# Kernel optimization log

Hardware: AMD Instinct MI355X
Metric: run time of the kernel (lower is better)

## Reference

```python
import jax, jax.numpy as jnp
import numpy as np

N_NODES = 100000
N_EDGES = 1600000
HID = 128
MAX_Z = 1000
N_GRAPHS = 1000
N_LAYERS = 3


def setup_inputs() -> dict:
    key = jax.random.key(0)
    ks = jax.random.split(key, 10)
    z = jax.random.randint(ks[0], (N_NODES,), 0, MAX_Z)
    edge_index = jax.random.randint(ks[1], (2, N_EDGES), 0, N_NODES)
    batch = jnp.sort(jax.random.randint(ks[2], (N_NODES,), 0, N_GRAPHS))
    s = 1.0 / np.sqrt(HID)
    z_emb = jax.random.normal(ks[3], (MAX_Z, HID), jnp.float32)
    Wl = jax.random.normal(ks[4], (N_LAYERS, HID, HID), jnp.float32) * s
    bl = jnp.zeros((N_LAYERS, HID), jnp.float32)
    Wr = jax.random.normal(ks[5], (N_LAYERS, HID, HID), jnp.float32) * s
    lin1_w = jax.random.normal(ks[6], (HID, HID), jnp.float32) * s
    lin1_b = jnp.zeros((HID,), jnp.float32)
    lin2_w = jax.random.normal(ks[7], (1, HID), jnp.float32) * s
    lin2_b = jnp.zeros((1,), jnp.float32)
    return dict(z=z, edge_index=edge_index, batch=batch, num_graphs=N_GRAPHS,
                z_emb=z_emb, Wl=Wl, bl=bl, Wr=Wr,
                lin1_w=lin1_w, lin1_b=lin1_b, lin2_w=lin2_w, lin2_b=lin2_b)


def _sage_conv(x, src, dst, deg_inv, Wl_i, bl_i, Wr_i):
    # PyG SAGEConv (default): out = lin_l(mean_{j in N(i)} x_j) + lin_r(x_i)
    agg = jax.ops.segment_sum(x[src], dst, num_segments=x.shape[0]) * deg_inv[:, None]
    return agg @ Wl_i.T + bl_i + x @ Wr_i.T


def reference(z, edge_index, batch, num_graphs, z_emb, Wl, bl, Wr, lin1_w, lin1_b, lin2_w, lin2_b):
    x = z_emb[z]  # z.ndim == 1 -> z_emb.ndim == 2, no sum branch
    src, dst = edge_index[0], edge_index[1]
    n = x.shape[0]
    deg = jax.ops.segment_sum(jnp.ones((src.shape[0],), x.dtype), dst, num_segments=n)
    deg_inv = 1.0 / jnp.maximum(deg, 1.0)  # mean aggregation; empty neighborhoods -> 0
    for i in range(Wl.shape[0] - 1):
        x = jax.nn.relu(_sage_conv(x, src, dst, deg_inv, Wl[i], bl[i], Wr[i]))
        # dropout is identity in eval mode
    x = _sage_conv(x, src, dst, deg_inv, Wl[-1], bl[-1], Wr[-1])
    # batch is sorted; first occurrence of each graph id == searchsorted
    center = jnp.searchsorted(batch, jnp.arange(num_graphs))
    h = x[center] * x[center + 1]
    h = jax.nn.relu(h @ lin1_w.T + lin1_b)
    return h @ lin2_w.T + lin2_b  # [num_graphs, 1]
```

## Files before the change

### kernel.cpp

```cpp
#include <hip/hip_runtime.h>
#include <hip/hip_bf16.h>
#include <cstdint>

#define HID 128
#define GM 128
#define SCAN_CHUNK 2048
#define NBIN 512
#define CHUNK 2048
#define MAXHI 1024

typedef __attribute__((ext_vector_type(8))) short bf16x8;
typedef __attribute__((ext_vector_type(4))) float f32x4;

__device__ __forceinline__ unsigned short f2bf(float f) {
    union { __hip_bfloat16 h; unsigned short u; } c;
    c.h = __float2bfloat16(f);
    return c.u;
}
__device__ __forceinline__ float bf2f(unsigned short u) {
    union { unsigned int i; float f; } c;
    c.i = ((unsigned int)u) << 16;
    return c.f;
}
__device__ __forceinline__ unsigned int pack2(unsigned short a, unsigned short b) {
    return (unsigned int)a | ((unsigned int)b << 16);
}
__device__ __forceinline__ bf16x8 ld_frag(const unsigned int* p) {
    union { uint4 u; bf16x8 f; } c;
    c.u = *(const uint4*)p;
    return c.f;
}

__device__ __forceinline__ int block_scan_excl(int v, int t, int* wtot, int* tot) {
    int lane = t & 63, wv = t >> 6;
    int incl = v;
#pragma unroll
    for (int off = 1; off < 64; off <<= 1) {
        int u = __shfl_up(incl, off);
        if (lane >= off) incl += u;
    }
    if (lane == 63) wtot[wv] = incl;
    __syncthreads();
    int woff = 0;
    for (int w = 0; w < wv; ++w) woff += wtot[w];
    if (tot) *tot = wtot[0] + wtot[1] + wtot[2] + wtot[3];
    __syncthreads();
    return woff + incl - v;
}

__global__ __launch_bounds__(256) void k_hist(const int* __restrict__ dst,
                                              int* __restrict__ hist, int n_edges) {
    __shared__ int h[NBIN];
    int t = threadIdx.x;
    h[t] = 0; h[t + 256] = 0;
    __syncthreads();
    int base = blockIdx.x * CHUNK;
#pragma unroll
    for (int j = 0; j < CHUNK / 256; ++j) {
        int e = base + j * 256 + t;
        if (e < n_edges) atomicAdd(&h[dst[e] & (NBIN - 1)], 1);
    }
    __syncthreads();
    hist[(size_t)blockIdx.x * NBIN + t] = h[t];
    hist[(size_t)blockIdx.x * NBIN + t + 256] = h[t + 256];
}

__global__ __launch_bounds__(256) void k_colscan(int* __restrict__ hist,
                                                 int* __restrict__ bintotal, int B) {
    __shared__ int wtot[4];
    int k = blockIdx.x, t = threadIdx.x;
    int run = 0;
    for (int base = 0; base < B; base += 256) {
        int b = base + t;
        int v = (b < B) ? hist[(size_t)b * NBIN + k] : 0;
        int tot;
        int excl = block_scan_excl(v, t, wtot, &tot);
        if (b < B) hist[(size_t)b * NBIN + k] = run + excl;
        run += tot;
    }
    if (t == 0) bintotal[k] = run;
}

__global__ __launch_bounds__(256) void k_binbase(const int* __restrict__ bintotal,
                                                 int* __restrict__ binbase) {
    __shared__ int wtot[4];
    int t = threadIdx.x;
    int a0 = bintotal[2 * t], a1 = bintotal[2 * t + 1];
    int excl = block_scan_excl(a0 + a1, t, wtot, nullptr);
    binbase[2 * t] = excl;
    binbase[2 * t + 1] = excl + a0;
    if (t == 255) binbase[NBIN] = excl + a0 + a1;
}

__global__ __launch_bounds__(256) void k_route(const int* __restrict__ src,
                                               const int* __restrict__ dst,
                                               const int* __restrict__ histex,
                                               const int* __restrict__ binbase,
                                               int2* __restrict__ ebuf, int n_edges) {
    __shared__ int h2[NBIN];
    __shared__ int basel[NBIN];
    int t = threadIdx.x;
    h2[t] = 0; h2[t + 256] = 0;
    basel[t]       = binbase[t]       + histex[(size_t)blockIdx.x * NBIN + t];
    basel[t + 256] = binbase[t + 256] + histex[(size_t)blockIdx.x * NBIN + t + 256];
    __syncthreads();
    int base = blockIdx.x * CHUNK;
#pragma unroll
    for (int j = 0; j < CHUNK / 256; ++j) {
        int e = base + j * 256 + t;
        if (e < n_edges) {
            int d = dst[e], s = src[e];
            int bin = d & (NBIN - 1);
            int r = atomicAdd(&h2[bin], 1);
            ebuf[basel[bin] + r] = make_int2(s, d);
        }
    }
}

__global__ __launch_bounds__(256) void k_group(const int2* __restrict__ ebuf,
                                               const int* __restrict__ binbase,
                                               const int* __restrict__ z,
                                               int2* __restrict__ csr2,
                                               int* __restrict__ start, int* __restrict__ deg,
                                               int n_nodes) {
    __shared__ int hh[MAXHI];
    __shared__ int cur[MAXHI];
    __shared__ int wtot[4];
    int k = blockIdx.x, t = threadIdx.x;
    int rs = binbase[k], re = binbase[k + 1];
#pragma unroll
    for (int j = 0; j < MAXHI / 256; ++j) hh[t + j * 256] = 0;
    __syncthreads();
    for (int i = rs + t; i < re; i += 256)
        atomicAdd(&hh[ebuf[i].y >> 9], 1);
    __syncthreads();
    int idx = t * 4;
    int a0 = hh[idx], a1 = hh[idx + 1], a2 = hh[idx + 2], a3 = hh[idx + 3];
    int excl = block_scan_excl(a0 + a1 + a2 + a3, t, wtot, nullptr);
    int e0 = excl, e1 = e0 + a0, e2 = e1 + a1, e3 = e2 + a2;
    cur[idx] = e0; cur[idx + 1] = e1; cur[idx + 2] = e2; cur[idx + 3] = e3;
    int ee[4] = {e0, e1, e2, e3};
    int aa[4] = {a0, a1, a2, a3};
#pragma unroll
    for (int j = 0; j < 4; ++j) {
        int node = ((idx + j) << 9) | k;
        if (node < n_nodes) {
            start[node] = rs + ee[j];
            deg[node] = aa[j];
        }
    }
    __syncthreads();
    for (int i = rs + t; i < re; i += 256) {
        int2 sd = ebuf[i];
        int r = atomicAdd(&cur[sd.y >> 9], 1);
        csr2[rs + r] = make_int2(sd.x, z[sd.x]);
    }
}

__global__ void k_scan1(const int* __restrict__ v_in, int* __restrict__ partials, int n) {
    __shared__ int sm[256];
    int t = threadIdx.x;
    int base = blockIdx.x * SCAN_CHUNK + t * 8;
    int s = 0;
#pragma unroll
    for (int j = 0; j < 8; ++j) { int i = base + j; if (i < n) s += v_in[i]; }
    sm[t] = s;
    __syncthreads();
    for (int off = 128; off > 0; off >>= 1) {
        if (t < off) sm[t] += sm[t + off];
        __syncthreads();
    }
    if (t == 0) partials[blockIdx.x] = sm[0];
}

__global__ void k_scan2(int* partials, int nchunks, int* total) {
    int lane = threadIdx.x;
    int v = (lane < nchunks) ? partials[lane] : 0;
#pragma unroll
    for (int off = 1; off < 64; off <<= 1) {
        int u = __shfl_up(v, off);
        if (lane >= off) v += u;
    }
    if (total && lane == nchunks - 1) *total = v;
    int ex = __shfl_up(v, 1);
    if (lane == 0) ex = 0;
    if (lane < nchunks) partials[lane] = ex;
}

__global__ void k_compact(const int* __restrict__ flag, const int* __restrict__ partials,
                          int* __restrict__ remap, int* __restrict__ nodes2, int n) {
    __shared__ int wtot[4];
    int t = threadIdx.x;
    int lane = t & 63, wv = t >> 6;
    int base = blockIdx.x * SCAN_CHUNK + t * 8;
    int v[8];
    int ts = 0;
#pragma unroll
    for (int j = 0; j < 8; ++j) { int i = base + j; v[j] = (i < n) ? flag[i] : 0; ts += v[j]; }
    int incl = ts;
#pragma unroll
    for (int off = 1; off < 64; off <<= 1) {
        int u = __shfl_up(incl, off);
        if (lane >= off) incl += u;
    }
    if (lane == 63) wtot[wv] = incl;
    __syncthreads();
    int woff = 0;
    for (int w = 0; w < wv; ++w) woff += wtot[w];
    int run = partials[blockIdx.x] + woff + (incl - ts);
#pragma unroll
    for (int j = 0; j < 8; ++j) {
        int i = base + j;
        if (i < n) {
            remap[i] = run;
            if (v[j]) nodes2[run] = i;
        }
        run += v[j];
    }
}

__global__ void k_zlr(const float* __restrict__ z_emb, const float* __restrict__ Wl,
                      const float* __restrict__ Wr, const float* __restrict__ bl,
                      float* __restrict__ zl, float* __restrict__ zr, int max_z) {
    __shared__ float row[HID];
    int r = blockIdx.x;
    if (r >= max_z) return;
    int t = threadIdx.x;
    if (t < HID) row[t] = z_emb[(size_t)r * HID + t];
    __syncthreads();
    int d = t & 127;
    const float* w = (t < 128 ? Wl : Wr) + (size_t)d * HID;
    float acc = 0.f;
#pragma unroll
    for (int k4 = 0; k4 < HID / 4; ++k4) {
        float4 wv = *(const float4*)(w + k4 * 4);
        float4 hv = *(const float4*)&row[k4 * 4];
        acc += wv.x * hv.x + wv.y * hv.y + wv.z * hv.z + wv.w * hv.w;
    }
    if (t < 128) zl[(size_t)r * HID + d] = acc;
    else         zr[(size_t)r * HID + d] = acc + bl[d];
}

__global__ void k_flag(const int* __restrict__ sel, const int* __restrict__ start,
                       const int* __restrict__ deg,
                       const int2* __restrict__ csr2, int* __restrict__ flag, int n_sel) {
    int r = (blockIdx.x * blockDim.x + threadIdx.x) >> 6;
    int lane = threadIdx.x & 63;
    if (r >= n_sel) return;
    int node = sel[r];
    if (lane == 0) flag[node] = 1;
    int s = start[node], e = s + deg[node];
    for (int i = s + lane; i < e; i += 64) flag[csr2[i].x] = 1;
}

__global__ void k_selremap(const int* __restrict__ sel, const int* __restrict__ remap,
                           int* __restrict__ selr, int n_sel) {
    int i = blockIdx.x * blockDim.x + threadIdx.x;
    if (i < n_sel) selr[i] = remap[sel[i]];
}

template<int MODE>
__global__ __launch_bounds__(256) void k_agg(const float* __restrict__ xv_,
                      float* __restrict__ aggout,
                      const int* __restrict__ start, const int* __restrict__ deg,
                      const int2* __restrict__ csr2,
                      const int* __restrict__ idxmap, const int* __restrict__ remap,
                      const int* __restrict__ z, const float* __restrict__ zr,
                      int n_host, const int* __restrict__ n_dev) {
    int nw_total = gridDim.x * 4;
    int w0 = blockIdx.x * 4 + (threadIdx.x >> 6);
    int lane = threadIdx.x & 63;
    int n = n_dev ? *n_dev : n_host;
    int half = lane >> 5;
    int col = lane & 31;
    const float4* xv = (const float4*)xv_;
    for (int r = w0; r < n; r += nw_total) {
        int node = (MODE == 1) ? r : idxmap[r];
        int s = start[node];
        int dg = deg[node];
        int e = s + dg;
        float4 a0 = {0.f,0.f,0.f,0.f}, a1 = {0.f,0.f,0.f,0.f};
        float4 a2 = {0.f,0.f,0.f,0.f}, a3 = {0.f,0.f,0.f,0.f};
        int i = s + half;
        for (; i + 6 < e; i += 8) {
            int2 c0 = csr2[i];
            int2 c1 = csr2[i + 2];
            int2 c2 = csr2[i + 4];
            int2 c3 = csr2[i + 6];
            int s0 = (MODE == 1) ? c0.y : c0.x;
            int s1 = (MODE == 1) ? c1.y : c1.x;
            int s2 = (MODE == 1) ? c2.y : c2.x;
            int s3 = (MODE == 1) ? c3.y : c3.x;
            if (MODE == 3) { s0 = remap[s0]; s1 = remap[s1]; s2 = remap[s2]; s3 = remap[s3]; }
            float4 v0 = xv[(size_t)s0 * 32 + col];
            float4 v1 = xv[(size_t)s1 * 32 + col];
            float4 v2 = xv[(size_t)s2 * 32 + col];
            float4 v3 = xv[(size_t)s3 * 32 + col];
            a0.x += v0.x; a0.y += v0.y; a0.z += v0.z; a0.w += v0.w;
            a1.x += v1.x; a1.y += v1.y; a1.z += v1.z; a1.w += v1.w;
            a2.x += v2.x; a2.y += v2.y; a2.z += v2.z; a2.w += v2.w;
            a3.x += v3.x; a3.y += v3.y; a3.z += v3.z; a3.w += v3.w;
        }
        for (; i < e; i += 2) {
            int2 c0 = csr2[i];
            int s0 = (MODE == 1) ? c0.y : c0.x;
            if (MODE == 3) s0 = remap[s0];
            float4 v0 = xv[(size_t)s0 * 32 + col];
            a0.x += v0.x; a0.y += v0.y; a0.z += v0.z; a0.w += v0.w;
        }
        a0.x += a1.x + a2.x + a3.x;
        a0.y += a1.y + a2.y + a3.y;
        a0.z += a1.z + a2.z + a3.z;
        a0.w += a1.w + a2.w + a3.w;
        a0.x += __shfl_xor(a0.x, 32);
        a0.y += __shfl_xor(a0.y, 32);
        a0.z += __shfl_xor(a0.z, 32);
        a0.w += __shfl_xor(a0.w, 32);
        if (half == 0) {
            float di = 1.0f / fmaxf((float)dg, 1.0f);
            float4 o = make_float4(a0.x * di, a0.y * di, a0.z * di, a0.w * di);
            if (MODE == 1) {
                int zn = z[node];
                float4 rv = ((const float4*)zr)[(size_t)zn * 32 + col];
                o.x = fmaxf(o.x + rv.x, 0.f);
                o.y = fmaxf(o.y + rv.y, 0.f);
                o.z = fmaxf(o.z + rv.z, 0.f);
                o.w = fmaxf(o.w + rv.w, 0.f);
            }
            ((float4*)aggout)[(size_t)r * 32 + col] = o;
        }
    }
}

__global__ void k_wsplit(const float* __restrict__ Wl, const float* __restrict__ Wr,
                         unsigned short* __restrict__ wh, unsigned short* __restrict__ wlo) {
    int idx = blockIdx.x * blockDim.x + threadIdx.x;
    if (idx >= 3 * HID * 2 * HID) return;
    int l = idx / (HID * 2 * HID);
    int r = idx - l * (HID * 2 * HID);
    int d = r >> 8;
    int k = r & 255;
    float v = (k < HID) ? Wl[((size_t)l * HID + d) * HID + k]
                        : Wr[((size_t)l * HID + d) * HID + (k - HID)];
    unsigned short h = f2bf(v);
    unsigned short lo = f2bf(v - bf2f(h));
    wh[idx] = h;
    wlo[idx] = lo;
}

__global__ __launch_bounds__(256) void k_gemm(const float* __restrict__ aggsrc,
                                              const float* __restrict__ xsrc,
                                              float* __restrict__ out,
                                              const unsigned short* __restrict__ wh,
                                              const unsigned short* __restrict__ wlo,
                                              const float* __restrict__ bias,
                                              const int* __restrict__ xidx,
                                              int n_host, const int* __restrict__ n_dev,
                                              int do_relu) {
    __shared__ unsigned int sAh[GM * 16], sAl[GM * 16];
    __shared__ unsigned int sBh[HID * 16], sBl[HID * 16];
    int n_rows = n_dev ? *n_dev : n_host;
    int t = threadIdx.x;
    int node0 = blockIdx.x * GM;
    if (node0 >= n_rows) return;
    int wv = t >> 6, lane = t & 63;
    int lrow = lane & 15, lk = lane >> 4;

    f32x4 acc[2][8];
#pragma unroll
    for (int m = 0; m < 2; ++m)
#pragma unroll
        for (int n = 0; n < 8; ++n) acc[m][n] = (f32x4){0.f, 0.f, 0.f, 0.f};

    int srow = t >> 2;
    int sq = t & 3;

    int gg[2] = {node0 + srow, node0 + srow + 64};
    bool vv[2] = {gg[0] < n_rows, gg[1] < n_rows};
    int xr[2];
#pragma unroll
    for (int rr = 0; rr < 2; ++rr)
        xr[rr] = xidx ? (vv[rr] ? xidx[gg[rr]] : 0) : gg[rr];

    for (int c = 0; c < 8; ++c) {
        int kbase = (c & 3) * 32;
        int kb = c * 32;
#pragma unroll
        for (int rr = 0; rr < 2; ++rr) {
            int row = srow + rr * 64;
            const float* srcrow = (c < 4) ? aggsrc + (size_t)gg[rr] * HID
                                          : xsrc + (size_t)xr[rr] * HID;
            float f[8];
            if (vv[rr]) {
                const float4* rp = (const float4*)(srcrow + kbase + sq * 8);
                float4 v0 = rp[0], v1 = rp[1];
                f[0]=v0.x; f[1]=v0.y; f[2]=v0.z; f[3]=v0.w;
                f[4]=v1.x; f[5]=v1.y; f[6]=v1.z; f[7]=v1.w;
            } else {
#pragma unroll
                for (int j = 0; j < 8; ++j) f[j] = 0.f;
            }
            unsigned int h[4], l[4];
#pragma unroll
            for (int j = 0; j < 4; ++j) {
                unsigned short h0 = f2bf(f[2*j]), h1 = f2bf(f[2*j+1]);
                unsigned short l0 = f2bf(f[2*j] - bf2f(h0));
                unsigned short l1 = f2bf(f[2*j+1] - bf2f(h1));
                h[j] = pack2(h0, h1);
                l[j] = pack2(l0, l1);
            }
            unsigned int base = row * 16 + sq * 4;
            *(uint4*)&sAh[base] = make_uint4(h[0], h[1], h[2], h[3]);
            *(uint4*)&sAl[base] = make_uint4(l[0], l[1], l[2], l[3]);
        }
#pragma unroll
        for (int rr = 0; rr < 2; ++rr) {
            int d = srow + rr * 64;
            size_t go = (size_t)d * 256 + kb + sq * 8;
            uint4 vh = *(const uint4*)(wh + go);
            uint4 vl = *(const uint4*)(wlo + go);
            unsigned int base = d * 16 + sq * 4;
            *(uint4*)&sBh[base] = vh;
            *(uint4*)&sBl[base] = vl;
        }
        __syncthreads();
        bf16x8 ah0, al0, ah1, al1;
        {
            unsigned int a0 = (unsigned)(wv * 32 + lrow) * 16 + lk * 4;
            unsigned int a1 = (unsigned)(wv * 32 + 16 + lrow) * 16 + lk * 4;
            ah0 = ld_frag(&sAh[a0]); al0 = ld_frag(&sAl[a0]);
            ah1 = ld_frag(&sAh[a1]); al1 = ld_frag(&sAl[a1]);
        }
#pragma unroll
        for (int n = 0; n < 8; ++n) {
            unsigned int b = (unsigned)(n * 16 + lrow) * 16 + lk * 4;
            bf16x8 bh = ld_frag(&sBh[b]);
            bf16x8 bl = ld_frag(&sBl[b]);
            acc[0][n] = __builtin_amdgcn_mfma_f32_16x16x32_bf16(ah0, bh, acc[0][n], 0, 0, 0);
            acc[0][n] = __builtin_amdgcn_mfma_f32_16x16x32_bf16(al0, bh, acc[0][n], 0, 0, 0);
            acc[0][n] = __builtin_amdgcn_mfma_f32_16x16x32_bf16(ah0, bl, acc[0][n], 0, 0, 0);
            acc[1][n] = __builtin_amdgcn_mfma_f32_16x16x32_bf16(ah1, bh, acc[1][n], 0, 0, 0);
            acc[1][n] = __builtin_amdgcn_mfma_f32_16x16x32_bf16(al1, bh, acc[1][n], 0, 0, 0);
            acc[1][n] = __builtin_amdgcn_mfma_f32_16x16x32_bf16(ah1, bl, acc[1][n], 0, 0, 0);
        }
        __syncthreads();
    }
#pragma unroll
    for (int m = 0; m < 2; ++m) {
        int rbase = node0 + wv * 32 + m * 16 + lk * 4;
#pragma unroll
        for (int n = 0; n < 8; ++n) {
            int colb = n * 16 + lrow;
            float bb = bias[colb];
#pragma unroll
            for (int r = 0; r < 4; ++r) {
                int row = rbase + r;
                if (row < n_rows) {
                    float v = acc[m][n][r] + bb;
                    if (do_relu) v = fmaxf(v, 0.f);
                    out[(size_t)row * HID + colb] = v;
                }
            }
        }
    }
}

__global__ void k_center(const int* __restrict__ batch, int* __restrict__ sel,
                         int n_nodes, int n_graphs) {
    int g = blockIdx.x * blockDim.x + threadIdx.x;
    if (g >= n_graphs) return;
    int lo = 0, hi = n_nodes;
    while (lo < hi) {
        int mid = (lo + hi) >> 1;
        if (batch[mid] < g) lo = mid + 1;
        else hi = mid;
    }
    sel[2 * g]     = min(lo, n_nodes - 1);
    sel[2 * g + 1] = min(lo + 1, n_nodes - 1);
}

__global__ void k_readout(const float* __restrict__ y,
                          const float* __restrict__ w1, const float* __restrict__ b1,
                          const float* __restrict__ w2, const float* __restrict__ b2,
                          float* __restrict__ out, int n_graphs) {
    __shared__ float h[HID];
    int g = blockIdx.x;
    if (g >= n_graphs) return;
    int lane = threadIdx.x;
    float2 a = ((const float2*)(y + (size_t)(2 * g) * HID))[lane];
    float2 b = ((const float2*)(y + (size_t)(2 * g + 1) * HID))[lane];
    h[2 * lane] = a.x * b.x;
    h[2 * lane + 1] = a.y * b.y;
    __syncthreads();
    int d0 = 2 * lane;
    float acc0 = b1[d0], acc1 = b1[d0 + 1];
    const float4* w1a = (const float4*)(w1 + (size_t)d0 * HID);
    const float4* w1b = (const float4*)(w1 + (size_t)(d0 + 1) * HID);
#pragma unroll 8
    for (int k4 = 0; k4 < HID / 4; ++k4) {
        float4 hv = *(const float4*)&h[k4 * 4];
        float4 wa = w1a[k4];
        float4 wb = w1b[k4];
        acc0 += hv.x * wa.x + hv.y * wa.y + hv.z * wa.z + hv.w * wa.w;
        acc1 += hv.x * wb.x + hv.y * wb.y + hv.z * wb.z + hv.w * wb.w;
    }
    float p = fmaxf(acc0, 0.f) * w2[d0] + fmaxf(acc1, 0.f) * w2[d0 + 1];
#pragma unroll
    for (int off = 32; off > 0; off >>= 1) p += __shfl_down(p, off);
    if (lane == 0) out[g] = p + b2[0];
}

extern "C" void kernel_launch(void* const* d_in, const int* in_sizes, int n_in,
                              void* d_out, int out_size, void* d_ws, size_t ws_size,
                              hipStream_t stream) {
    const int* z = (const int*)d_in[0];
    const int* edge_index = (const int*)d_in[1];
    const int* batch = (const int*)d_in[2];
    const float* z_emb = (const float*)d_in[4];
    const float* Wl = (const float*)d_in[5];
    const float* bl = (const float*)d_in[6];
    const float* Wr = (const float*)d_in[7];
    const float* lin1_w = (const float*)d_in[8];
    const float* lin1_b = (const float*)d_in[9];
    const float* lin2_w = (const float*)d_in[10];
    const float* lin2_b = (const float*)d_in[11];
    float* out = (float*)d_out;

    int n_nodes = in_sizes[0];
    int n_edges = in_sizes[1] / 2;
    int max_z = in_sizes[4] / HID;
    int n_graphs = out_size;
    int n_sel = 2 * n_graphs;

    const int* e_src = edge_index;
    const int* e_dst = edge_index + n_edges;

    char* p = (char*)d_ws;
    auto alloc = [&](size_t bytes) {
        char* r = p;
        p += (bytes + 511) & ~(size_t)511;
        return r;
    };
    float* x      = (float*)alloc((size_t)n_nodes * HID * 4);
    float* agg2   = (float*)alloc((size_t)n_nodes * HID * 4);
    float* x2c    = (float*)alloc((size_t)n_nodes * HID * 4);
    float* aggsel = (float*)alloc((size_t)n_sel * HID * 4);
    float* y      = (float*)alloc((size_t)n_sel * HID * 4);
    int*   deg    = (int*)alloc((size_t)n_nodes * 4);
    int*   start  = (int*)alloc((size_t)n_nodes * 4);
    int2*  ebuf   = (int2*)alloc((size_t)n_edges * 8);
    int2*  csr2   = (int2*)alloc((size_t)n_edges * 8);
    int B = (n_edges + CHUNK - 1) / CHUNK;
    int*   hist     = (int*)alloc((size_t)B * NBIN * 4);
    int*   bintotal = (int*)alloc((size_t)NBIN * 4);
    int*   binbase  = (int*)alloc((size_t)(NBIN + 1) * 4);
    int*   parts  = (int*)alloc(64 * 4);
    int*   sel    = (int*)alloc((size_t)n_sel * 4);
    int*   selr   = (int*)alloc((size_t)n_sel * 4);
    int*   flag   = (int*)alloc((size_t)n_nodes * 4);
    int*   remap  = (int*)alloc((size_t)n_nodes * 4);
    int*   nodes2 = (int*)alloc((size_t)n_nodes * 4);
    int*   n2     = (int*)alloc(4);
    float* zl     = (float*)alloc((size_t)max_z * HID * 4);
    float* zr     = (float*)alloc((size_t)max_z * HID * 4);
    unsigned short* wh  = (unsigned short*)alloc((size_t)3 * HID * 2 * HID * 2);
    unsigned short* wlo = (unsigned short*)alloc((size_t)3 * HID * 2 * HID * 2);

    hipMemsetAsync(flag, 0, (size_t)n_nodes * 4, stream);

    k_wsplit<<<(3 * HID * 2 * HID + 255) / 256, 256, 0, stream>>>(Wl, Wr, wh, wlo);
    k_zlr<<<max_z, 256, 0, stream>>>(z_emb, Wl, Wr, bl, zl, zr, max_z);

    k_hist<<<B, 256, 0, stream>>>(e_dst, hist, n_edges);
    k_colscan<<<NBIN, 256, 0, stream>>>(hist, bintotal, B);
    k_binbase<<<1, 256, 0, stream>>>(bintotal, binbase);
    k_route<<<B, 256, 0, stream>>>(e_src, e_dst, hist, binbase, ebuf, n_edges);
    k_group<<<NBIN, 256, 0, stream>>>(ebuf, binbase, z, csr2, start, deg, n_nodes);

    k_center<<<(n_graphs + 255) / 256, 256, 0, stream>>>(batch, sel, n_nodes, n_graphs);

    k_flag<<<(n_sel * 64 + 255) / 256, 256, 0, stream>>>(sel, start, deg, csr2, flag, n_sel);
    int nchunks = (n_nodes + SCAN_CHUNK - 1) / SCAN_CHUNK;
    k_scan1<<<nchunks, 256, 0, stream>>>(flag, parts, n_nodes);
    k_scan2<<<1, 64, 0, stream>>>(parts, nchunks, n2);
    k_compact<<<nchunks, 256, 0, stream>>>(flag, parts, remap, nodes2, n_nodes);
    k_selremap<<<(n_sel + 255) / 256, 256, 0, stream>>>(sel, remap, selr, n_sel);

    int agg_blocks = (n_nodes + 3) / 4;
    k_agg<1><<<agg_blocks, 256, 0, stream>>>(zl, x, start, deg, csr2, nullptr,
                                             nullptr, z, zr, n_nodes, nullptr);
    k_agg<2><<<2048, 256, 0, stream>>>(x, agg2, start, deg, csr2, nodes2,
                                       nullptr, nullptr, nullptr, 0, n2);
    k_gemm<<<(n_nodes + GM - 1) / GM, 256, 0, stream>>>(agg2, x, x2c,
                                            wh + (size_t)HID * 2 * HID,
                                            wlo + (size_t)HID * 2 * HID,
                                            bl + HID, nodes2, 0, n2, 1);
    k_agg<3><<<(n_sel + 3) / 4, 256, 0, stream>>>(x2c, aggsel, start, deg, csr2, sel,
                                                  remap, nullptr, nullptr, n_sel, nullptr);
    k_gemm<<<(n_sel + GM - 1) / GM, 256, 0, stream>>>(aggsel, x2c, y,
                                                      wh + (size_t)2 * HID * 2 * HID,
                                                      wlo + (size_t)2 * HID * 2 * HID,
                                                      bl + (size_t)2 * HID,
                                                      selr, n_sel, nullptr, 0);
    k_readout<<<n_graphs, 64, 0, stream>>>(y, lin1_w, lin1_b, lin2_w, lin2_b, out, n_graphs);
}
```

Before: 261.6 us.

## Split CSR into src and precomputed z-offset arrays, merge prep kernels, rework layer-1 gather

The interleaved int2 CSR becomes two int arrays, the source index and a byte offset into the z-embedding table (z<<9). Layer-1 aggregation can then read 4 bytes per edge and address rows without a multiply, and it now issues 8 predicated loads at a time so more memory requests are in flight. The weight-split and z-projection kernels are merged into one launch, and the selremap kernel is removed by having the final GEMM apply remap itself. This cuts launch count and edge-index bandwidth, but adds masked redundant loads at the tail of each neighbour list.

Result: no change. 263.6 us (+0.8%).

```diff
diff --git a/kernel.cpp b/kernel.cpp
--- a/kernel.cpp
+++ b/kernel.cpp
@@ -120,7 +120,8 @@
 __global__ __launch_bounds__(256) void k_group(const int2* __restrict__ ebuf,
                                                const int* __restrict__ binbase,
                                                const int* __restrict__ z,
-                                               int2* __restrict__ csr2,
+                                               int* __restrict__ csr_src,
+                                               int* __restrict__ csr_zoff,
                                                int* __restrict__ start, int* __restrict__ deg,
                                                int n_nodes) {
     __shared__ int hh[MAXHI];
@@ -152,8 +153,9 @@
     __syncthreads();
     for (int i = rs + t; i < re; i += 256) {
         int2 sd = ebuf[i];
-        int r = atomicAdd(&cur[sd.y >> 9], 1);
-        csr2[rs + r] = make_int2(sd.x, z[sd.x]);
+        int r = rs + atomicAdd(&cur[sd.y >> 9], 1);
+        csr_src[r] = sd.x;
+        csr_zoff[r] = z[sd.x] << 9;
     }
 }
 
@@ -219,51 +221,61 @@
     }
 }
 
-__global__ void k_zlr(const float* __restrict__ z_emb, const float* __restrict__ Wl,
-                      const float* __restrict__ Wr, const float* __restrict__ bl,
-                      float* __restrict__ zl, float* __restrict__ zr, int max_z) {
-    __shared__ float row[HID];
-    int r = blockIdx.x;
-    if (r >= max_z) return;
+__global__ void k_prep(const float* __restrict__ z_emb, const float* __restrict__ Wl,
+                       const float* __restrict__ Wr, const float* __restrict__ bl,
+                       float* __restrict__ zl, float* __restrict__ zr,
+                       unsigned short* __restrict__ wh, unsigned short* __restrict__ wlo,
+                       int max_z) {
     int t = threadIdx.x;
-    if (t < HID) row[t] = z_emb[(size_t)r * HID + t];
-    __syncthreads();
-    int d = t & 127;
-    const float* w = (t < 128 ? Wl : Wr) + (size_t)d * HID;
-    float acc = 0.f;
-#pragma unroll
-    for (int k4 = 0; k4 < HID / 4; ++k4) {
-        float4 wv = *(const float4*)(w + k4 * 4);
-        float4 hv = *(const float4*)&row[k4 * 4];
-        acc += wv.x * hv.x + wv.y * hv.y + wv.z * hv.z + wv.w * hv.w;
-    }
-    if (t < 128) zl[(size_t)r * HID + d] = acc;
-    else         zr[(size_t)r * HID + d] = acc + bl[d];
+    if ((int)blockIdx.x < max_z) {
+        __shared__ float row[HID];
+        int r = blockIdx.x;
+        if (t < HID) row[t] = z_emb[(size_t)r * HID + t];
+        __syncthreads();
+        int d = t & 127;
+        const float* w = (t < 128 ? Wl : Wr) + (size_t)d * HID;
+        float acc = 0.f;
+#pragma unroll
+        for (int k4 = 0; k4 < HID / 4; ++k4) {
+            float4 wv = *(const float4*)(w + k4 * 4);
+            float4 hv = *(const float4*)&row[k4 * 4];
+            acc += wv.x * hv.x + wv.y * hv.y + wv.z * hv.z + wv.w * hv.w;
+        }
+        if (t < 128) zl[(size_t)r * HID + d] = acc;
+        else         zr[(size_t)r * HID + d] = acc + bl[d];
+    } else {
+        int idx = (blockIdx.x - max_z) * 256 + t;
+        if (idx >= 3 * HID * 2 * HID) return;
+        int l = idx / (HID * 2 * HID);
+        int r = idx - l * (HID * 2 * HID);
+        int d = r >> 8;
+        int k = r & 255;
+        float v = (k < HID) ? Wl[((size_t)l * HID + d) * HID + k]
+                            : Wr[((size_t)l * HID + d) * HID + (k - HID)];
+        unsigned short h = f2bf(v);
+        unsigned short lo = f2bf(v - bf2f(h));
+        wh[idx] = h;
+        wlo[idx] = lo;
+    }
 }
 
 __global__ void k_flag(const int* __restrict__ sel, const int* __restrict__ start,
                        const int* __restrict__ deg,
-                       const int2* __restrict__ csr2, int* __restrict__ flag, int n_sel) {
+                       const int* __restrict__ csr_src, int* __restrict__ flag, int n_sel) {
     int r = (blockIdx.x * blockDim.x + threadIdx.x) >> 6;
     int lane = threadIdx.x & 63;
     if (r >= n_sel) return;
     int node = sel[r];
     if (lane == 0) flag[node] = 1;
     int s = start[node], e = s + deg[node];
-    for (int i = s + lane; i < e; i += 64) flag[csr2[i].x] = 1;
-}
-
-__global__ void k_selremap(const int* __restrict__ sel, const int* __restrict__ remap,
-                           int* __restrict__ selr, int n_sel) {
-    int i = blockIdx.x * blockDim.x + threadIdx.x;
-    if (i < n_sel) selr[i] = remap[sel[i]];
+    for (int i = s + lane; i < e; i += 64) flag[csr_src[i]] = 1;
 }
 
 template<int MODE>
 __global__ __launch_bounds__(256) void k_agg(const float* __restrict__ xv_,
                       float* __restrict__ aggout,
                       const int* __restrict__ start, const int* __restrict__ deg,
-                      const int2* __restrict__ csr2,
+                      const int* __restrict__ csr_src, const int* __restrict__ csr_zoff,
                       const int* __restrict__ idxmap, const int* __restrict__ remap,
                       const int* __restrict__ z, const float* __restrict__ zr,
                       int n_host, const int* __restrict__ n_dev) {
@@ -274,44 +286,65 @@
     int half = lane >> 5;
     int col = lane & 31;
     const float4* xv = (const float4*)xv_;
+    const char* xc = (const char*)xv_;
     for (int r = w0; r < n; r += nw_total) {
         int node = (MODE == 1) ? r : idxmap[r];
         int s = start[node];
         int dg = deg[node];
         int e = s + dg;
-        float4 a0 = {0.f,0.f,0.f,0.f}, a1 = {0.f,0.f,0.f,0.f};
-        float4 a2 = {0.f,0.f,0.f,0.f}, a3 = {0.f,0.f,0.f,0.f};
-        int i = s + half;
-        for (; i + 6 < e; i += 8) {
-            int2 c0 = csr2[i];
-            int2 c1 = csr2[i + 2];
-            int2 c2 = csr2[i + 4];
-            int2 c3 = csr2[i + 6];
-            int s0 = (MODE == 1) ? c0.y : c0.x;
-            int s1 = (MODE == 1) ? c1.y : c1.x;
-            int s2 = (MODE == 1) ? c2.y : c2.x;
-            int s3 = (MODE == 1) ? c3.y : c3.x;
-            if (MODE == 3) { s0 = remap[s0]; s1 = remap[s1]; s2 = remap[s2]; s3 = remap[s3]; }
-            float4 v0 = xv[(size_t)s0 * 32 + col];
-            float4 v1 = xv[(size_t)s1 * 32 + col];
-            float4 v2 = xv[(size_t)s2 * 32 + col];
-            float4 v3 = xv[(size_t)s3 * 32 + col];
-            a0.x += v0.x; a0.y += v0.y; a0.z += v0.z; a0.w += v0.w;
-            a1.x += v1.x; a1.y += v1.y; a1.z += v1.z; a1.w += v1.w;
-            a2.x += v2.x; a2.y += v2.y; a2.z += v2.z; a2.w += v2.w;
-            a3.x += v3.x; a3.y += v3.y; a3.z += v3.z; a3.w += v3.w;
-        }
-        for (; i < e; i += 2) {
-            int2 c0 = csr2[i];
-            int s0 = (MODE == 1) ? c0.y : c0.x;
-            if (MODE == 3) s0 = remap[s0];
-            float4 v0 = xv[(size_t)s0 * 32 + col];
-            a0.x += v0.x; a0.y += v0.y; a0.z += v0.z; a0.w += v0.w;
-        }
-        a0.x += a1.x + a2.x + a3.x;
-        a0.y += a1.y + a2.y + a3.y;
-        a0.z += a1.z + a2.z + a3.z;
-        a0.w += a1.w + a2.w + a3.w;
+        float4 a0 = {0.f,0.f,0.f,0.f};
+        if (MODE == 1) {
+            for (int i = s + half; i < e; i += 16) {
+                int off[8];
+                float msk[8];
+#pragma unroll
+                for (int k = 0; k < 8; ++k) {
+                    int p = i + 2 * k;
+                    bool valid = p < e;
+                    off[k] = csr_zoff[valid ? p : e - 1];
+                    msk[k] = valid ? 1.f : 0.f;
+                }
+                float4 v[8];
+#pragma unroll
+                for (int k = 0; k < 8; ++k)
+                    v[k] = ((const float4*)(xc + off[k]))[col];
+#pragma unroll
+                for (int k = 0; k < 8; ++k) {
+                    a0.x = fmaf(v[k].x, msk[k], a0.x);
+                    a0.y = fmaf(v[k].y, msk[k], a0.y);
+                    a0.z = fmaf(v[k].z, msk[k], a0.z);
+                    a0.w = fmaf(v[k].w, msk[k], a0.w);
+                }
+            }
+        } else {
+            float4 a1 = {0.f,0.f,0.f,0.f}, a2 = {0.f,0.f,0.f,0.f}, a3 = {0.f,0.f,0.f,0.f};
+            int i = s + half;
+            for (; i + 6 < e; i += 8) {
+                int s0 = csr_src[i];
+                int s1 = csr_src[i + 2];
+                int s2 = csr_src[i + 4];
+                int s3 = csr_src[i + 6];
+                if (MODE == 3) { s0 = remap[s0]; s1 = remap[s1]; s2 = remap[s2]; s3 = remap[s3]; }
+                float4 v0 = xv[(size_t)s0 * 32 + col];
+                float4 v1 = xv[(size_t)s1 * 32 + col];
+                float4 v2 = xv[(size_t)s2 * 32 + col];
+                float4 v3 = xv[(size_t)s3 * 32 + col];
+                a0.x += v0.x; a0.y += v0.y; a0.z += v0.z; a0.w += v0.w;
+                a1.x += v1.x; a1.y += v1.y; a1.z += v1.z; a1.w += v1.w;
+                a2.x += v2.x; a2.y += v2.y; a2.z += v2.z; a2.w += v2.w;
+                a3.x += v3.x; a3.y += v3.y; a3.z += v3.z; a3.w += v3.w;
+            }
+            for (; i < e; i += 2) {
+                int s0 = csr_src[i];
+                if (MODE == 3) s0 = remap[s0];
+                float4 v0 = xv[(size_t)s0 * 32 + col];
+                a0.x += v0.x; a0.y += v0.y; a0.z += v0.z; a0.w += v0.w;
+            }
+            a0.x += a1.x + a2.x + a3.x;
+            a0.y += a1.y + a2.y + a3.y;
+            a0.z += a1.z + a2.z + a3.z;
+            a0.w += a1.w + a2.w + a3.w;
+        }
         a0.x += __shfl_xor(a0.x, 32);
         a0.y += __shfl_xor(a0.y, 32);
         a0.z += __shfl_xor(a0.z, 32);
@@ -332,22 +365,6 @@
     }
 }
 
-__global__ void k_wsplit(const float* __restrict__ Wl, const float* __restrict__ Wr,
-                         unsigned short* __restrict__ wh, unsigned short* __restrict__ wlo) {
-    int idx = blockIdx.x * blockDim.x + threadIdx.x;
-    if (idx >= 3 * HID * 2 * HID) return;
-    int l = idx / (HID * 2 * HID);
-    int r = idx - l * (HID * 2 * HID);
-    int d = r >> 8;
-    int k = r & 255;
-    float v = (k < HID) ? Wl[((size_t)l * HID + d) * HID + k]
-                        : Wr[((size_t)l * HID + d) * HID + (k - HID)];
-    unsigned short h = f2bf(v);
-    unsigned short lo = f2bf(v - bf2f(h));
-    wh[idx] = h;
-    wlo[idx] = lo;
-}
-
 __global__ __launch_bounds__(256) void k_gemm(const float* __restrict__ aggsrc,
                                               const float* __restrict__ xsrc,
                                               float* __restrict__ out,
@@ -355,6 +372,7 @@
                                               const unsigned short* __restrict__ wlo,
                                               const float* __restrict__ bias,
                                               const int* __restrict__ xidx,
+                                              const int* __restrict__ remap2,
                                               int n_host, const int* __restrict__ n_dev,
                                               int do_relu) {
     __shared__ unsigned int sAh[GM * 16], sAl[GM * 16];
@@ -379,8 +397,10 @@
     bool vv[2] = {gg[0] < n_rows, gg[1] < n_rows};
     int xr[2];
 #pragma unroll
-    for (int rr = 0; rr < 2; ++rr)
-        xr[rr] = xidx ? (vv[rr] ? xidx[gg[rr]] : 0) : gg[rr];
+    for (int rr = 0; rr < 2; ++rr) {
+        int v = xidx ? (vv[rr] ? xidx[gg[rr]] : 0) : gg[rr];
+        xr[rr] = remap2 ? remap2[v] : v;
+    }
 
     for (int c = 0; c < 8; ++c) {
         int kbase = (c & 3) * 32;
@@ -541,22 +561,22 @@
         p += (bytes + 511) & ~(size_t)511;
         return r;
     };
-    float* x      = (float*)alloc((size_t)n_nodes * HID * 4);
-    float* agg2   = (float*)alloc((size_t)n_nodes * HID * 4);
-    float* x2c    = (float*)alloc((size_t)n_nodes * HID * 4);
-    float* aggsel = (float*)alloc((size_t)n_sel * HID * 4);
-    float* y      = (float*)alloc((size_t)n_sel * HID * 4);
-    int*   deg    = (int*)alloc((size_t)n_nodes * 4);
-    int*   start  = (int*)alloc((size_t)n_nodes * 4);
-    int2*  ebuf   = (int2*)alloc((size_t)n_edges * 8);
-    int2*  csr2   = (int2*)alloc((size_t)n_edges * 8);
+    float* x       = (float*)alloc((size_t)n_nodes * HID * 4);
+    float* agg2    = (float*)alloc((size_t)n_nodes * HID * 4);
+    float* x2c     = (float*)alloc((size_t)n_nodes * HID * 4);
+    float* aggsel  = (float*)alloc((size_t)n_sel * HID * 4);
+    float* y       = (float*)alloc((size_t)n_sel * HID * 4);
+    int*   deg     = (int*)alloc((size_t)n_nodes * 4);
+    int*   start   = (int*)alloc((size_t)n_nodes * 4);
+    int2*  ebuf    = (int2*)alloc((size_t)n_edges * 8);
+    int*   csr_src = (int*)alloc((size_t)n_edges * 4);
+    int*   csr_zoff= (int*)alloc((size_t)n_edges * 4);
     int B = (n_edges + CHUNK - 1) / CHUNK;
     int*   hist     = (int*)alloc((size_t)B * NBIN * 4);
     int*   bintotal = (int*)alloc((size_t)NBIN * 4);
     int*   binbase  = (int*)alloc((size_t)(NBIN + 1) * 4);
     int*   parts  = (int*)alloc(64 * 4);
     int*   sel    = (int*)alloc((size_t)n_sel * 4);
-    int*   selr   = (int*)alloc((size_t)n_sel * 4);
     int*   flag   = (int*)alloc((size_t)n_nodes * 4);
     int*   remap  = (int*)alloc((size_t)n_nodes * 4);
     int*   nodes2 = (int*)alloc((size_t)n_nodes * 4);
@@ -568,39 +588,38 @@
 
     hipMemsetAsync(flag, 0, (size_t)n_nodes * 4, stream);
 
-    k_wsplit<<<(3 * HID * 2 * HID + 255) / 256, 256, 0, stream>>>(Wl, Wr, wh, wlo);
-    k_zlr<<<max_z, 256, 0, stream>>>(z_emb, Wl, Wr, bl, zl, zr, max_z);
+    int wsplit_blocks = (3 * HID * 2 * HID + 255) / 256;
+    k_prep<<<max_z + wsplit_blocks, 256, 0, stream>>>(z_emb, Wl, Wr, bl, zl, zr, wh, wlo, max_z);
 
     k_hist<<<B, 256, 0, stream>>>(e_dst, hist, n_edges);
     k_colscan<<<NBIN, 256, 0, stream>>>(hist, bintotal, B);
     k_binbase<<<1, 256, 0, stream>>>(bintotal, binbase);
     k_route<<<B, 256, 0, stream>>>(e_src, e_dst, hist, binbase, ebuf, n_edges);
-    k_group<<<NBIN, 256, 0, stream>>>(ebuf, binbase, z, csr2, start, deg, n_nodes);
+    k_group<<<NBIN, 256, 0, stream>>>(ebuf, binbase, z, csr_src, csr_zoff, start, deg, n_nodes);
 
     k_center<<<(n_graphs + 255) / 256, 256, 0, stream>>>(batch, sel, n_nodes, n_graphs);
 
-    k_flag<<<(n_sel * 64 + 255) / 256, 256, 0, stream>>>(sel, start, deg, csr2, flag, n_sel);
+    k_flag<<<(n_sel * 64 + 255) / 256, 256, 0, stream>>>(sel, start, deg, csr_src, flag, n_sel);
     int nchunks = (n_nodes + SCAN_CHUNK - 1) / SCAN_CHUNK;
     k_scan1<<<nchunks, 256, 0, stream>>>(flag, parts, n_nodes);
     k_scan2<<<1, 64, 0, stream>>>(parts, nchunks, n2);
     k_compact<<<nchunks, 256, 0, stream>>>(flag, parts, remap, nodes2, n_nodes);
-    k_selremap<<<(n_sel + 255) / 256, 256, 0, stream>>>(sel, remap, selr, n_sel);
 
     int agg_blocks = (n_nodes + 3) / 4;
-    k_agg<1><<<agg_blocks, 256, 0, stream>>>(zl, x, start, deg, csr2, nullptr,
-                                             nullptr, z, zr, n_nodes, nullptr);
-    k_agg<2><<<2048, 256, 0, stream>>>(x, agg2, start, deg, csr2, nodes2,
+    k_agg<1><<<agg_blocks, 256, 0, stream>>>(zl, x, start, deg, csr_src, csr_zoff,
+                                             nullptr, nullptr, z, zr, n_nodes, nullptr);
+    k_agg<2><<<2048, 256, 0, stream>>>(x, agg2, start, deg, csr_src, nullptr, nodes2,
                                        nullptr, nullptr, nullptr, 0, n2);
     k_gemm<<<(n_nodes + GM - 1) / GM, 256, 0, stream>>>(agg2, x, x2c,
                                             wh + (size_t)HID * 2 * HID,
                                             wlo + (size_t)HID * 2 * HID,
-                                            bl + HID, nodes2, 0, n2, 1);
-    k_agg<3><<<(n_sel + 3) / 4, 256, 0, stream>>>(x2c, aggsel, start, deg, csr2, sel,
-                                                  remap, nullptr, nullptr, n_sel, nullptr);
+                                            bl + HID, nodes2, nullptr, 0, n2, 1);
+    k_agg<3><<<(n_sel + 3) / 4, 256, 0, stream>>>(x2c, aggsel, start, deg, csr_src, nullptr,
+                                                  sel, remap, nullptr, nullptr, n_sel, nullptr);
     k_gemm<<<(n_sel + GM - 1) / GM, 256, 0, stream>>>(aggsel, x2c, y,
                                                       wh + (size_t)2 * HID * 2 * HID,
                                                       wlo + (size_t)2 * HID * 2 * HID,
                                                       bl + (size_t)2 * HID,
-                                                      selr, n_sel, nullptr, 0);
+                                                      sel, remap, n_sel, nullptr, 0);
     k_readout<<<n_graphs, 64, 0, stream>>>(y, lin1_w, lin1_b, lin2_w, lin2_b, out, n_graphs);
 }
```
